# Performance work log

Measured on AMD Instinct MI355X. Metric: run time of the kernel, lower is better.

The kernel has to match this reference:

```python
import jax, jax.numpy as jnp
import numpy as np

BETA = 0.25


def setup_inputs() -> dict:
    key = jax.random.key(0)
    k1, k2, k3, k4 = jax.random.split(key, 4)
    n_emb, emb_dim, in_ch = 16384, 256, 1024
    feats = jax.random.normal(k1, (8, in_ch, 32, 32), dtype=jnp.float32)
    conv_w = jax.random.normal(k2, (emb_dim, in_ch), dtype=jnp.float32) * (1.0 / np.sqrt(in_ch))
    conv_b = jax.random.normal(k3, (emb_dim,), dtype=jnp.float32) * 0.01
    # torch init: uniform(-1/n_emb, 1/n_emb)
    codebook = jax.random.uniform(k4, (n_emb, emb_dim), dtype=jnp.float32,
                                  minval=-1.0 / n_emb, maxval=1.0 / n_emb)
    return {"feats": feats, "conv_w": conv_w, "conv_b": conv_b, "codebook": codebook}


def reference(feats, conv_w, conv_b, codebook):
    sg = jax.lax.stop_gradient
    # 1x1 conv == channel GEMM: [B,C,H,W] -> [B,E,H,W]
    z = jnp.einsum('bchw,ec->behw', feats, conv_w) + conv_b[None, :, None, None]
    z = jnp.transpose(z, (0, 2, 3, 1))            # [B,H,W,E]
    B, H, W, E = z.shape
    zf = z.reshape(-1, E)                          # [N,E]
    # pairwise squared distances: ||z||^2 + ||e||^2 - 2 z.e^T
    d = (jnp.sum(zf * zf, axis=1, keepdims=True)
         + jnp.sum(codebook * codebook, axis=1)
         - 2.0 * zf @ codebook.T)                  # [N,n_emb]
    idx = jnp.argmin(d, axis=1)                    # [N]
    # one-hot matmul in original == direct gather (same math)
    z_q = codebook[idx].reshape(B, H, W, E)
    loss = jnp.mean((sg(z_q) - z) ** 2) + BETA * jnp.mean((z_q - sg(z)) ** 2)
    z_q = z + sg(z_q - z)                          # straight-through
    z_q = jnp.transpose(z_q, (0, 3, 1, 2))         # [B,E,H,W]
    return (z_q, loss)
```

## Files before the change

kernel.cpp:

```cpp
#include <hip/hip_runtime.h>
#include <hip/hip_bf16.h>
#include <stdint.h>


typedef float f32x4 __attribute__((ext_vector_type(4)));
typedef int i32x4 __attribute__((ext_vector_type(4)));
typedef int i32x16 __attribute__((ext_vector_type(16)));
typedef short s16x8 __attribute__((ext_vector_type(8)));

__device__ __forceinline__ void gl2lds16(const void* g, void* l) {
  __builtin_amdgcn_global_load_lds(
      (const __attribute__((address_space(1))) void*)g,
      (__attribute__((address_space(3))) void*)l, 16, 0, 0);
}

__device__ __forceinline__ unsigned short f2bf(float f) {
  unsigned u = __float_as_uint(f);
  u = u + 0x7FFFu + ((u >> 16) & 1u);
  return (unsigned short)(u >> 16);
}
__device__ __forceinline__ float bf2f(unsigned short u) {
  return __uint_as_float(((unsigned)u) << 16);
}

__device__ __forceinline__ ushort4 cvt4(float4 v) {
  ushort4 o;
  o.x = f2bf(v.x); o.y = f2bf(v.y); o.z = f2bf(v.z); o.w = f2bf(v.w);
  return o;
}

__global__ void k_prep(const float* __restrict__ cbk, const float* __restrict__ Wsrc,
                       const float* __restrict__ feats,
                       signed char* __restrict__ cbs8, unsigned short* __restrict__ W2,
                       unsigned short* __restrict__ At, float* __restrict__ lossw,
                       int* __restrict__ best) {
  __shared__ float tile[64][65];
  int blk = blockIdx.x, t = threadIdx.x;
  if (blk == 0 && t < 2) ((int*)lossw)[t] = 0;
  if (blk < 8) {
    #pragma unroll
    for (int k = 0; k < 4; ++k) best[blk * 1024 + k * 256 + t] = (int)0x80000000;
  }
  if (blk < 256) {
    int jt = blk;
    #pragma unroll
    for (int lp = 0; lp < 4; ++lp) {
      int fl = lp * 256 + t;
      int ks = fl >> 7, fr = (fl >> 6) & 1, lane = fl & 63;
      int j = jt * 64 + fr * 32 + (lane & 31);
      int k = ks * 32 + (lane >> 5) * 16;
      const float* src = cbk + (size_t)j * 256 + k;
      int w4[4];
      #pragma unroll
      for (int q4 = 0; q4 < 4; ++q4) {
        float4 v = *(const float4*)(src + q4 * 4);
        int b0 = __float2int_rn(v.x * 2080768.0f);
        int b1 = __float2int_rn(v.y * 2080768.0f);
        int b2 = __float2int_rn(v.z * 2080768.0f);
        int b3 = __float2int_rn(v.w * 2080768.0f);
        w4[q4] = (b0 & 255) | ((b1 & 255) << 8) | ((b2 & 255) << 16) | ((b3 & 255) << 24);
      }
      int4* dst = (int4*)(cbs8 + (size_t)jt * 16384 + (size_t)fl * 16);
      *dst = make_int4(w4[0], w4[1], w4[2], w4[3]);
    }
  } else if (blk < 384) {
    size_t base = (size_t)(blk - 256) * 2048 + t * 8;
    float4 v0 = *(const float4*)(Wsrc + base);
    float4 v1 = *(const float4*)(Wsrc + base + 4);
    *(ushort4*)(W2 + base) = cvt4(v0);
    *(ushort4*)(W2 + base + 4) = cvt4(v1);
  } else {
    int id = blk - 384;
    int b = id >> 8, c0 = ((id >> 4) & 15) * 64, s0 = (id & 15) * 64;
    int tc = t >> 4, ts = (t & 15) * 4;
    #pragma unroll
    for (int k = 0; k < 4; ++k) {
      float4 v = *(const float4*)(feats + ((size_t)b * 1024 + c0 + tc + k * 16) * 1024 + s0 + ts);
      tile[tc + k * 16][ts] = v.x;
      tile[tc + k * 16][ts + 1] = v.y;
      tile[tc + k * 16][ts + 2] = v.z;
      tile[tc + k * 16][ts + 3] = v.w;
    }
    __syncthreads();
    #pragma unroll
    for (int k = 0; k < 4; ++k) {
      int sr = tc + k * 16;
      float4 v;
      v.x = tile[ts][sr]; v.y = tile[ts + 1][sr];
      v.z = tile[ts + 2][sr]; v.w = tile[ts + 3][sr];
      *(ushort4*)(At + (size_t)(b * 1024 + s0 + sr) * 1024 + c0 + ts) = cvt4(v);
    }
  }
}

__global__ __launch_bounds__(256, 2)
void k_gemm1(const unsigned short* __restrict__ At, const unsigned short* __restrict__ Bw,
             const float* __restrict__ bias, unsigned short* __restrict__ zb,
             signed char* __restrict__ z8) {
  __shared__ __align__(16) uint8_t lds[2048 * 16];
  uint8_t* ldsA = lds;
  uint8_t* ldsB = lds + 1024 * 16;
  const int t = threadIdx.x, w = t >> 6, l = t & 63;
  const int wy = w >> 1, wx = w & 1, l15 = l & 15, q = l >> 4;
  const int ib = blockIdx.y * 64, eb = blockIdx.x * 64;
  f32x4 acc[2][2] = {};
  for (int kt = 0; kt < 8; ++kt) {
    int c0 = kt * 128;
    __syncthreads();
    #pragma unroll
    for (int r = 0; r < 4; ++r) {
      int P = t + 256 * r;
      gl2lds16(At + (size_t)(ib + (P & 63)) * 1024 + c0 + (P >> 6) * 8, ldsA + P * 16);
    }
    #pragma unroll
    for (int r = 0; r < 4; ++r) {
      int P = t + 256 * r;
      gl2lds16(Bw + (size_t)(eb + (P & 63)) * 1024 + c0 + (P >> 6) * 8, ldsB + P * 16);
    }
    __syncthreads();
    #pragma unroll
    for (int s = 0; s < 4; ++s) {
      s16x8 a[2], b[2];
      #pragma unroll
      for (int fr = 0; fr < 2; ++fr)
        a[fr] = *(const s16x8*)(ldsA + ((s * 4 + q) * 64 + wy * 32 + fr * 16 + l15) * 16);
      #pragma unroll
      for (int fc = 0; fc < 2; ++fc)
        b[fc] = *(const s16x8*)(ldsB + ((s * 4 + q) * 64 + wx * 32 + fc * 16 + l15) * 16);
      #pragma unroll
      for (int fr = 0; fr < 2; ++fr)
        #pragma unroll
        for (int fc = 0; fc < 2; ++fc)
          acc[fr][fc] = __builtin_amdgcn_mfma_f32_16x16x32_bf16(a[fr], b[fc], acc[fr][fc], 0, 0, 0);
    }
  }
  #pragma unroll
  for (int fc = 0; fc < 2; ++fc) {
    int e = eb + wx * 32 + fc * 16 + l15;
    float bv = bias[e];
    #pragma unroll
    for (int fr = 0; fr < 2; ++fr)
      #pragma unroll
      for (int r = 0; r < 4; ++r) {
        int i = ib + wy * 32 + fr * 16 + q * 4 + r;
        float zf = acc[fr][fc][r] + bv;
        zb[(size_t)i * 256 + e] = f2bf(zf);
        int qv = __float2int_rn(zf * 16.0f);
        qv = qv > 127 ? 127 : (qv < -127 ? -127 : qv);
        z8[(size_t)i * 256 + e] = (signed char)qv;
      }
  }
}

__global__ __launch_bounds__(256, 2)
void k_gemm2(const signed char* __restrict__ cbs8, const signed char* __restrict__ z8,
             int* __restrict__ best) {
  __shared__ __align__(16) uint8_t ldsB[32768];
  __shared__ int csh[4][128];
  const int t = threadIdx.x, w = t >> 6, l = t & 63;
  const int l31 = l & 31, h = l >> 5;
  const int ib = blockIdx.y * 128;
  #pragma unroll
  for (int r = 0; r < 8; ++r) {
    int P = t + 256 * r;
    gl2lds16(z8 + (size_t)(ib + (P & 127)) * 256 + (P >> 7) * 16, ldsB + P * 16);
  }
  int ibest[4];
  #pragma unroll
  for (int fc = 0; fc < 4; ++fc) ibest[fc] = (int)0x80000000;
  __syncthreads();
  const uint8_t* bbase = ldsB + (h * 128 + l31) * 16;
  #pragma unroll 1
  for (int js = 0; js < 2; ++js) {
    const int jtile = blockIdx.x * 8 + js * 4 + w;
    const uint8_t* abase = (const uint8_t*)cbs8 + (size_t)jtile * 16384 + l * 16;
    i32x16 acc[2][4] = {};
    #pragma unroll 2
    for (int ks = 0; ks < 8; ++ks) {
      i32x4 a0 = *(const i32x4*)(abase + (ks * 2) * 1024);
      i32x4 a1 = *(const i32x4*)(abase + (ks * 2 + 1) * 1024);
      i32x4 b0 = *(const i32x4*)(bbase + ks * 4096);
      i32x4 b1 = *(const i32x4*)(bbase + ks * 4096 + 512);
      i32x4 b2 = *(const i32x4*)(bbase + ks * 4096 + 1024);
      i32x4 b3 = *(const i32x4*)(bbase + ks * 4096 + 1536);
      acc[0][0] = __builtin_amdgcn_mfma_i32_32x32x32_i8(a0, b0, acc[0][0], 0, 0, 0);
      acc[1][0] = __builtin_amdgcn_mfma_i32_32x32x32_i8(a1, b0, acc[1][0], 0, 0, 0);
      acc[0][1] = __builtin_amdgcn_mfma_i32_32x32x32_i8(a0, b1, acc[0][1], 0, 0, 0);
      acc[1][1] = __builtin_amdgcn_mfma_i32_32x32x32_i8(a1, b1, acc[1][1], 0, 0, 0);
      acc[0][2] = __builtin_amdgcn_mfma_i32_32x32x32_i8(a0, b2, acc[0][2], 0, 0, 0);
      acc[1][2] = __builtin_amdgcn_mfma_i32_32x32x32_i8(a1, b2, acc[1][2], 0, 0, 0);
      acc[0][3] = __builtin_amdgcn_mfma_i32_32x32x32_i8(a0, b3, acc[0][3], 0, 0, 0);
      acc[1][3] = __builtin_amdgcn_mfma_i32_32x32x32_i8(a1, b3, acc[1][3], 0, 0, 0);
    }
    const int cbase = 511 - js * 256;
    #pragma unroll
    for (int fc = 0; fc < 4; ++fc) {
      int bb = ibest[fc];
      #pragma unroll
      for (int fr = 0; fr < 2; ++fr) {
        const int c1 = cbase - fr * 32;
        #pragma unroll
        for (int rg = 0; rg < 16; rg += 2) {
          int c0 = c1 - ((rg & 3) + 8 * (rg >> 2));
          int p0 = (int)(((unsigned)acc[fr][fc][rg] << 9) + (unsigned)c0);
          int p1 = (int)(((unsigned)acc[fr][fc][rg + 1] << 9) + (unsigned)(c0 - 1));
          bb = max(max(p0, p1), bb);
        }
      }
      ibest[fc] = bb;
    }
  }
  const float inv = 1.0f / 33292288.0f;
  const int jbase = blockIdx.x * 512 + w * 64 + 4 * h;
  #pragma unroll
  for (int fc = 0; fc < 4; ++fc) {
    int p = ibest[fc];
    int accw = p >> 9;
    int loc = 511 - (p & 511);
    int j = jbase + loc;
    float s = fmaf((float)accw, inv, 3.0f);
    int gb = (int)(((unsigned)__float_as_int(s) << 14) + (unsigned)(16383 - j));
    int bb = max(gb, __shfl_xor(gb, 32, 64));
    if (l < 32) csh[w][fc * 32 + l31] = bb;
  }
  __syncthreads();
  if (t < 128) {
    int m0 = max(max(csh[0][t], csh[1][t]), max(csh[2][t], csh[3][t]));
    atomicMax(&best[ib + t], m0);
  }
}

__global__ void k_final(const float* __restrict__ cbk, const unsigned short* __restrict__ zb,
                        const int* __restrict__ best, float* __restrict__ lossw,
                        float* __restrict__ out) {
  __shared__ float tile[32][257];
  __shared__ int lidx[32];
  __shared__ float ps[4];
  int blk = blockIdx.x, t = threadIdx.x;
  int b = blk >> 5, s0 = (blk & 31) * 32;
  int gi0 = b * 1024 + s0;
  int r8 = t >> 3, c8 = t & 7;
  int bv = best[gi0 + r8];
  if (t < 32) lidx[t] = 16383 - (best[gi0 + t] & 0x3FFF);
  const unsigned short* zrow = zb + (size_t)(gi0 + r8) * 256 + c8 * 32;
  float ss = 0.0f;
  #pragma unroll
  for (int k = 0; k < 32; k += 4) {
    ushort4 v = *(const ushort4*)(zrow + k);
    float a0 = bf2f(v.x), a1 = bf2f(v.y), a2 = bf2f(v.z), a3 = bf2f(v.w);
    ss += a0 * a0 + a1 * a1 + a2 * a2 + a3 * a3;
  }
  ss += __shfl_xor(ss, 1, 64);
  ss += __shfl_xor(ss, 2, 64);
  ss += __shfl_xor(ss, 4, 64);
  float dist = 0.0f;
  if (c8 == 0) dist = ss - (float)(bv >> 14) * (1.0f / 1048576.0f);
  float v = dist;
  #pragma unroll
  for (int m = 32; m; m >>= 1) v += __shfl_down(v, m, 64);
  if ((t & 63) == 0) ps[t >> 6] = v;
  __syncthreads();
  if (t == 0) {
    float part = ps[0] + ps[1] + ps[2] + ps[3];
    atomicAdd(lossw, part);
    __threadfence();
    int cnt = atomicAdd((int*)lossw + 1, 1);
    if (cnt == 255) {
      __threadfence();
      float total = atomicAdd(lossw, 0.0f);
      out[2097152] = 1.25f * total * (1.0f / 2097152.0f);
    }
  }
  int w = t >> 6, l = t & 63;
  #pragma unroll
  for (int rr = 0; rr < 8; ++rr) {
    int r = w * 8 + rr;
    const float* src = cbk + (size_t)lidx[r] * 256;
    #pragma unroll
    for (int k = 0; k < 4; ++k)
      tile[r][l + 64 * k] = src[l + 64 * k];
  }
  __syncthreads();
  int sl = t & 31, eg = t >> 5;
  size_t ob = (size_t)b * 262144 + s0 + sl;
  #pragma unroll
  for (int k = 0; k < 32; ++k) {
    int e = eg + 8 * k;
    out[ob + (size_t)e * 1024] = tile[sl][e];
  }
}

extern "C" void kernel_launch(void* const* d_in, const int* in_sizes, int n_in,
                              void* d_out, int out_size, void* d_ws, size_t ws_size,
                              hipStream_t stream) {
  const float* feats  = (const float*)d_in[0];
  const float* conv_w = (const float*)d_in[1];
  const float* conv_b = (const float*)d_in[2];
  const float* cbk    = (const float*)d_in[3];
  float* out = (float*)d_out;
  char* ws = (char*)d_ws;
  unsigned short* featsT = (unsigned short*)(ws);
  unsigned short* W2     = (unsigned short*)(ws + 16777216);
  signed char*    cbs8   = (signed char*)(ws + 17301504);
  unsigned short* zb     = (unsigned short*)(ws + 21495808);
  signed char*    z8     = (signed char*)(ws + 25690112);
  int*            best   = (int*)(ws + 27787264);
  float*          lossw  = (float*)(ws + 27820032);

  k_prep<<<2432, 256, 0, stream>>>(cbk, conv_w, feats, cbs8, W2, featsT, lossw, best);
  k_gemm1<<<dim3(4, 128), 256, 0, stream>>>(featsT, W2, conv_b, zb, z8);
  k_gemm2<<<dim3(32, 64), 256, 0, stream>>>(cbs8, z8, best);
  k_final<<<256, 256, 0, stream>>>(cbk, zb, best, lossw, out);
}
```

Measured before the change: 162.7 us.

## Fuse feats transpose into GEMM1 load and compute row norms in epilogue

Drops the separate transpose-and-convert pass over feats in the prep kernel. GEMM1 now reads fp32 feats directly, converts them to bf16 and writes them into LDS in the layout it needs. The bf16 z buffer is removed: GEMM1 accumulates per-row squared norms into a zsq array with atomics, and the final kernel reads those norms instead of re-reading z. This cuts a full 16MB write plus re-read and a 4MB z buffer. In exchange, the GEMM1 A-tile load becomes synchronous scalar global loads instead of async global-to-LDS, and the epilogue adds atomics.

```diff
diff --git a/kernel.cpp b/kernel.cpp
--- a/kernel.cpp
+++ b/kernel.cpp
@@ -19,9 +19,6 @@
   u = u + 0x7FFFu + ((u >> 16) & 1u);
   return (unsigned short)(u >> 16);
 }
-__device__ __forceinline__ float bf2f(unsigned short u) {
-  return __uint_as_float(((unsigned)u) << 16);
-}
 
 __device__ __forceinline__ ushort4 cvt4(float4 v) {
   ushort4 o;
@@ -30,16 +27,17 @@
 }
 
 __global__ void k_prep(const float* __restrict__ cbk, const float* __restrict__ Wsrc,
-                       const float* __restrict__ feats,
                        signed char* __restrict__ cbs8, unsigned short* __restrict__ W2,
-                       unsigned short* __restrict__ At, float* __restrict__ lossw,
-                       int* __restrict__ best) {
-  __shared__ float tile[64][65];
+                       float* __restrict__ lossw, int* __restrict__ best,
+                       float* __restrict__ zsq) {
   int blk = blockIdx.x, t = threadIdx.x;
   if (blk == 0 && t < 2) ((int*)lossw)[t] = 0;
   if (blk < 8) {
     #pragma unroll
-    for (int k = 0; k < 4; ++k) best[blk * 1024 + k * 256 + t] = (int)0x80000000;
+    for (int k = 0; k < 4; ++k) {
+      best[blk * 1024 + k * 256 + t] = (int)0x80000000;
+      zsq[blk * 1024 + k * 256 + t] = 0.0f;
+    }
   }
   if (blk < 256) {
     int jt = blk;
@@ -63,54 +61,37 @@
       int4* dst = (int4*)(cbs8 + (size_t)jt * 16384 + (size_t)fl * 16);
       *dst = make_int4(w4[0], w4[1], w4[2], w4[3]);
     }
-  } else if (blk < 384) {
+  } else {
     size_t base = (size_t)(blk - 256) * 2048 + t * 8;
     float4 v0 = *(const float4*)(Wsrc + base);
     float4 v1 = *(const float4*)(Wsrc + base + 4);
     *(ushort4*)(W2 + base) = cvt4(v0);
     *(ushort4*)(W2 + base + 4) = cvt4(v1);
-  } else {
-    int id = blk - 384;
-    int b = id >> 8, c0 = ((id >> 4) & 15) * 64, s0 = (id & 15) * 64;
-    int tc = t >> 4, ts = (t & 15) * 4;
-    #pragma unroll
-    for (int k = 0; k < 4; ++k) {
-      float4 v = *(const float4*)(feats + ((size_t)b * 1024 + c0 + tc + k * 16) * 1024 + s0 + ts);
-      tile[tc + k * 16][ts] = v.x;
-      tile[tc + k * 16][ts + 1] = v.y;
-      tile[tc + k * 16][ts + 2] = v.z;
-      tile[tc + k * 16][ts + 3] = v.w;
-    }
-    __syncthreads();
-    #pragma unroll
-    for (int k = 0; k < 4; ++k) {
-      int sr = tc + k * 16;
-      float4 v;
-      v.x = tile[ts][sr]; v.y = tile[ts + 1][sr];
-      v.z = tile[ts + 2][sr]; v.w = tile[ts + 3][sr];
-      *(ushort4*)(At + (size_t)(b * 1024 + s0 + sr) * 1024 + c0 + ts) = cvt4(v);
-    }
   }
 }
 
 __global__ __launch_bounds__(256, 2)
-void k_gemm1(const unsigned short* __restrict__ At, const unsigned short* __restrict__ Bw,
-             const float* __restrict__ bias, unsigned short* __restrict__ zb,
-             signed char* __restrict__ z8) {
+void k_gemm1(const float* __restrict__ feats, const unsigned short* __restrict__ Bw,
+             const float* __restrict__ bias, signed char* __restrict__ z8,
+             float* __restrict__ zsq) {
   __shared__ __align__(16) uint8_t lds[2048 * 16];
   uint8_t* ldsA = lds;
   uint8_t* ldsB = lds + 1024 * 16;
   const int t = threadIdx.x, w = t >> 6, l = t & 63;
   const int wy = w >> 1, wx = w & 1, l15 = l & 15, q = l >> 4;
   const int ib = blockIdx.y * 64, eb = blockIdx.x * 64;
+  const int b1024 = (ib >> 10) * 1024, s0 = ib & 1023;
   f32x4 acc[2][2] = {};
   for (int kt = 0; kt < 8; ++kt) {
     int c0 = kt * 128;
     __syncthreads();
     #pragma unroll
-    for (int r = 0; r < 4; ++r) {
-      int P = t + 256 * r;
-      gl2lds16(At + (size_t)(ib + (P & 63)) * 1024 + c0 + (P >> 6) * 8, ldsA + P * 16);
+    for (int r = 0; r < 8; ++r) {
+      int csub = 4 * w + 16 * r;
+      const float* src = feats + (size_t)(b1024 + c0 + csub) * 1024 + s0 + l;
+      float4 v;
+      v.x = src[0]; v.y = src[1024]; v.z = src[2048]; v.w = src[3072];
+      *(ushort4*)(ldsA + ((csub >> 3) * 64 + l) * 16 + (csub & 4) * 2) = cvt4(v);
     }
     #pragma unroll
     for (int r = 0; r < 4; ++r) {
@@ -134,6 +115,7 @@
           acc[fr][fc] = __builtin_amdgcn_mfma_f32_16x16x32_bf16(a[fr], b[fc], acc[fr][fc], 0, 0, 0);
     }
   }
+  float zv[2][2][4];
   #pragma unroll
   for (int fc = 0; fc < 2; ++fc) {
     int e = eb + wx * 32 + fc * 16 + l15;
@@ -142,14 +124,26 @@
     for (int fr = 0; fr < 2; ++fr)
       #pragma unroll
       for (int r = 0; r < 4; ++r) {
+        float zf = acc[fr][fc][r] + bv;
+        zv[fc][fr][r] = zf;
         int i = ib + wy * 32 + fr * 16 + q * 4 + r;
-        float zf = acc[fr][fc][r] + bv;
-        zb[(size_t)i * 256 + e] = f2bf(zf);
         int qv = __float2int_rn(zf * 16.0f);
         qv = qv > 127 ? 127 : (qv < -127 ? -127 : qv);
         z8[(size_t)i * 256 + e] = (signed char)qv;
       }
   }
+  #pragma unroll
+  for (int fr = 0; fr < 2; ++fr)
+    #pragma unroll
+    for (int r = 0; r < 4; ++r) {
+      float p = zv[0][fr][r] * zv[0][fr][r] + zv[1][fr][r] * zv[1][fr][r];
+      p += __shfl_xor(p, 1, 64);
+      p += __shfl_xor(p, 2, 64);
+      p += __shfl_xor(p, 4, 64);
+      p += __shfl_xor(p, 8, 64);
+      if (l15 == 0)
+        atomicAdd(&zsq[ib + wy * 32 + fr * 16 + q * 4 + r], p);
+    }
 }
 
 __global__ __launch_bounds__(256, 2)
@@ -230,39 +224,29 @@
   }
 }
 
-__global__ void k_final(const float* __restrict__ cbk, const unsigned short* __restrict__ zb,
+__global__ void k_final(const float* __restrict__ cbk, const float* __restrict__ zsq,
                         const int* __restrict__ best, float* __restrict__ lossw,
                         float* __restrict__ out) {
   __shared__ float tile[32][257];
   __shared__ int lidx[32];
-  __shared__ float ps[4];
   int blk = blockIdx.x, t = threadIdx.x;
   int b = blk >> 5, s0 = (blk & 31) * 32;
   int gi0 = b * 1024 + s0;
-  int r8 = t >> 3, c8 = t & 7;
-  int bv = best[gi0 + r8];
-  if (t < 32) lidx[t] = 16383 - (best[gi0 + t] & 0x3FFF);
-  const unsigned short* zrow = zb + (size_t)(gi0 + r8) * 256 + c8 * 32;
-  float ss = 0.0f;
-  #pragma unroll
-  for (int k = 0; k < 32; k += 4) {
-    ushort4 v = *(const ushort4*)(zrow + k);
-    float a0 = bf2f(v.x), a1 = bf2f(v.y), a2 = bf2f(v.z), a3 = bf2f(v.w);
-    ss += a0 * a0 + a1 * a1 + a2 * a2 + a3 * a3;
-  }
-  ss += __shfl_xor(ss, 1, 64);
-  ss += __shfl_xor(ss, 2, 64);
-  ss += __shfl_xor(ss, 4, 64);
-  float dist = 0.0f;
-  if (c8 == 0) dist = ss - (float)(bv >> 14) * (1.0f / 1048576.0f);
-  float v = dist;
-  #pragma unroll
-  for (int m = 32; m; m >>= 1) v += __shfl_down(v, m, 64);
-  if ((t & 63) == 0) ps[t >> 6] = v;
-  __syncthreads();
+  float d = 0.0f;
+  if (t < 32) {
+    int bv = best[gi0 + t];
+    lidx[t] = 16383 - (bv & 0x3FFF);
+    d = zsq[gi0 + t] - (float)(bv >> 14) * (1.0f / 1048576.0f);
+  }
+  if (t < 64) {
+    d += __shfl_down(d, 16, 64);
+    d += __shfl_down(d, 8, 64);
+    d += __shfl_down(d, 4, 64);
+    d += __shfl_down(d, 2, 64);
+    d += __shfl_down(d, 1, 64);
+  }
   if (t == 0) {
-    float part = ps[0] + ps[1] + ps[2] + ps[3];
-    atomicAdd(lossw, part);
+    atomicAdd(lossw, d);
     __threadfence();
     int cnt = atomicAdd((int*)lossw + 1, 1);
     if (cnt == 255) {
@@ -271,6 +255,7 @@
       out[2097152] = 1.25f * total * (1.0f / 2097152.0f);
     }
   }
+  __syncthreads();
   int w = t >> 6, l = t & 63;
   #pragma unroll
   for (int rr = 0; rr < 8; ++rr) {
@@ -299,16 +284,15 @@
   const float* cbk    = (const float*)d_in[3];
   float* out = (float*)d_out;
   char* ws = (char*)d_ws;
-  unsigned short* featsT = (unsigned short*)(ws);
-  unsigned short* W2     = (unsigned short*)(ws + 16777216);
-  signed char*    cbs8   = (signed char*)(ws + 17301504);
-  unsigned short* zb     = (unsigned short*)(ws + 21495808);
-  signed char*    z8     = (signed char*)(ws + 25690112);
-  int*            best   = (int*)(ws + 27787264);
-  float*          lossw  = (float*)(ws + 27820032);
-
-  k_prep<<<2432, 256, 0, stream>>>(cbk, conv_w, feats, cbs8, W2, featsT, lossw, best);
-  k_gemm1<<<dim3(4, 128), 256, 0, stream>>>(featsT, W2, conv_b, zb, z8);
+  unsigned short* W2    = (unsigned short*)(ws);
+  signed char*    cbs8  = (signed char*)(ws + 524288);
+  signed char*    z8    = (signed char*)(ws + 4718592);
+  int*            best  = (int*)(ws + 6815744);
+  float*          zsq   = (float*)(ws + 6848512);
+  float*          lossw = (float*)(ws + 6881280);
+
+  k_prep<<<384, 256, 0, stream>>>(cbk, conv_w, cbs8, W2, lossw, best, zsq);
+  k_gemm1<<<dim3(4, 128), 256, 0, stream>>>(feats, W2, conv_b, z8, zsq);
   k_gemm2<<<dim3(32, 64), 256, 0, stream>>>(cbs8, z8, best);
-  k_final<<<256, 256, 0, stream>>>(cbk, zb, best, lossw, out);
-}
+  k_final<<<256, 256, 0, stream>>>(cbk, zsq, best, lossw, out);
+}
```

After: 164.6 us. Within noise of the previous version (+1.2%).
